# Performance work log

Measured on AMD Instinct MI355X. Metric: run time of the kernel, lower is better.

Reference implementation:

```python
import jax, jax.numpy as jnp
import numpy as np

L, T, F, DIM = 16, 16384, 2, 3
N_MIN, N_MAX = 16.0, 512.0
N_PTS = 262144
# torch code builds np.int32 primes [1, 2654435761, 805459861]; 2654435761 wraps to -1640531535.
# Since T is a power of two, int32 wraparound multiply/xor followed by nonnegative mod T gives
# bit-identical indices to the int64 torch computation.
PIS = jnp.array([1, -1640531535, 805459861], dtype=jnp.int32)
# corner ordering from get_indices: corner k = a*4+b*2+c with a->dim0, b->dim1, c->dim2
OFFS = jnp.array([[(k >> 2) & 1, (k >> 1) & 1, k & 1] for k in range(8)], dtype=jnp.float32)  # (8,3)


def setup_inputs() -> dict:
    key = jax.random.key(0)
    k1, k2 = jax.random.split(key)
    x = jax.random.uniform(k1, (N_PTS, DIM), dtype=jnp.float32)
    # nn.init.uniform_(weight, a=-1e-4, b=1e-4) for each of L tables of shape (T, F)
    embeddings = jax.random.uniform(k2, (L, T, F), minval=-1e-4, maxval=1e-4, dtype=jnp.float32)
    return {"x": x, "embeddings": embeddings}


def reference(x, embeddings):
    # per-level growth factor b = exp((log Nmax - log Nmin)/L); N_l = Nmin * b**l
    b = jnp.exp((jnp.log(N_MAX) - jnp.log(N_MIN)) / L)
    N_l = N_MIN * b ** jnp.arange(L, dtype=jnp.float32)                      # (L,)
    un_x = x[None, :, :] * N_l[:, None, None]                                # (L,N,3)  (mu=0, sigma=1)
    lo = jnp.floor(un_x)
    hi = jnp.ceil(un_x)
    d = hi - lo                                                              # (L,N,3)
    nz = d != 0
    diff = jnp.where(nz, (un_x - lo) / jnp.where(nz, d, 1.0), 0.0)           # (L,N,3)

    mask = OFFS.astype(bool)[None, None]                                     # (1,1,8,3)
    corners = jnp.where(mask, hi[:, :, None, :], lo[:, :, None, :])          # (L,N,8,3)
    ci = corners.astype(jnp.int32)
    prod = ci * PIS                                                          # (L,N,8,3) wrapping int32 mul
    idx = jnp.mod(prod[..., 0] ^ prod[..., 1] ^ prod[..., 2], T)             # (L,N,8)

    # per-level table gather: (L,T,F)[ (L,N,8) ] -> (L,N,8,F)
    feats = jax.vmap(lambda emb, i: emb[i])(embeddings, idx)

    # trilinear weights: prod over dims of (diff if corner bit else 1-diff)
    w = jnp.prod(jnp.where(mask, diff[:, :, None, :], 1.0 - diff[:, :, None, :]), axis=-1)  # (L,N,8)
    c = jnp.einsum('lnc,lncf->lnf', w, feats)                                # (L,N,F)
    return jnp.transpose(c, (1, 0, 2)).reshape(x.shape[0], L * F)            # (N, L*F)
```

## Files before the change

kernel.cpp:

```cpp
#include <hip/hip_runtime.h>
#include <stdint.h>

constexpr int L_LEVELS = 16;
constexpr int T_SIZE   = 16384;
constexpr int N_PTS    = 262144;

typedef _Float16 h2 __attribute__((ext_vector_type(2)));
typedef _Float16 h4 __attribute__((ext_vector_type(4)));
typedef _Float16 h8 __attribute__((ext_vector_type(8)));

constexpr uint32_t P1_4 = 2654435761u * 4u;
constexpr uint32_t P2_4 = 805459861u * 4u;
constexpr uint32_t M4   = (T_SIZE - 1) * 4u;

__device__ __forceinline__ h2 lerp2(h2 a, h2 b, h2 t) {
    return a + t * (b - a);
}

__global__ __launch_bounds__(256) void cvt_emb(
    const float4* __restrict__ src, h4* __restrict__ dst)
{
    const int i = blockIdx.x * 256 + threadIdx.x;
    const float4 v = src[i];
    h4 w = { (_Float16)v.x, (_Float16)v.y, (_Float16)v.z, (_Float16)v.w };
    dst[i] = w;
}

__global__ __launch_bounds__(1024, 4) void hash_encode_pair(
    const float* __restrict__ x,
    const h2* __restrict__ emb16,
    h2* __restrict__ ws)
{
    __shared__ h2 tab[2][T_SIZE];

    const int lp    = blockIdx.x & 7;
    const int chunk = blockIdx.x >> 3;
    const int t     = threadIdx.x;
    const int n0    = chunk * 8192 + t * 8;

    {
        const float4* __restrict__ sA =
            reinterpret_cast<const float4*>(emb16 + (size_t)lp * T_SIZE);
        const float4* __restrict__ sB =
            reinterpret_cast<const float4*>(emb16 + (size_t)(lp + 8) * T_SIZE);
        float4* __restrict__ dA = reinterpret_cast<float4*>(tab[0]);
        float4* __restrict__ dB = reinterpret_cast<float4*>(tab[1]);
#pragma unroll
        for (int it = 0; it < 4; ++it) {
            dA[it * 1024 + t] = sA[it * 1024 + t];
            dB[it * 1024 + t] = sB[it * 1024 + t];
        }
    }

    union { float4 q[6]; float f[24]; } xs;
    {
        const float4* __restrict__ xv =
            reinterpret_cast<const float4*>(x + (size_t)n0 * 3);
#pragma unroll
        for (int i = 0; i < 6; ++i) xs.q[i] = xv[i];
    }

    __syncthreads();

#pragma unroll 1
    for (int s = 0; s < 2; ++s) {
        const int lv = lp + 8 * s;
        const float Nl = 16.0f * exp2f((float)lv * 0.3125f);
        const char* __restrict__ tb = reinterpret_cast<const char*>(tab[s]);

        union { h2 r[8]; float4 q[2]; } res;

#pragma unroll
        for (int p = 0; p < 8; ++p) {
            const float u0 = xs.f[3 * p + 0] * Nl;
            const float u1 = xs.f[3 * p + 1] * Nl;
            const float u2 = xs.f[3 * p + 2] * Nl;

            const float fl0 = floorf(u0), fl1 = floorf(u1), fl2 = floorf(u2);
            const float df0 = u0 - fl0, df1 = u1 - fl1, df2 = u2 - fl2;

            const uint32_t q0 = ((uint32_t)(int32_t)fl0) << 2;
            const uint32_t q1 = ((uint32_t)(int32_t)fl1) * P1_4;
            const uint32_t q2 = ((uint32_t)(int32_t)fl2) * P2_4;
            const uint32_t d0 = (q0 ^ (q0 + 4u))   & M4;
            const uint32_t d1 = (q1 ^ (q1 + P1_4)) & M4;
            const uint32_t d2 = (q2 ^ (q2 + P2_4)) & M4;

            uint32_t off = (q0 ^ q1 ^ q2) & M4;

            constexpr int gray[8] = {0, 1, 3, 2, 6, 7, 5, 4};
            h2 f[8];
#pragma unroll
            for (int j = 0; j < 8; ++j) {
                f[gray[j]] = *reinterpret_cast<const h2*>(tb + off);
                if (j < 7) {
                    const int tog = gray[j] ^ gray[j + 1];
                    off ^= (tog == 4) ? d0 : (tog == 2) ? d1 : d2;
                }
            }

            const _Float16 h0 = (_Float16)df0, h1 = (_Float16)df1,
                           hz = (_Float16)df2;
            const h2 t0 = {h0, h0}, t1 = {h1, h1}, t2 = {hz, hz};
            h2 e0 = lerp2(f[0], f[1], t2);
            h2 e1 = lerp2(f[2], f[3], t2);
            h2 e2 = lerp2(f[4], f[5], t2);
            h2 e3 = lerp2(f[6], f[7], t2);
            h2 g0 = lerp2(e0, e1, t1);
            h2 g1 = lerp2(e2, e3, t1);
            res.r[p] = lerp2(g0, g1, t0);
        }

        float4* ws4 = reinterpret_cast<float4*>(ws + (size_t)lv * N_PTS + n0);
        ws4[0] = res.q[0];
        ws4[1] = res.q[1];
    }
}

__global__ __launch_bounds__(256) void transpose_lnf_nlf(
    const h2* __restrict__ ws,
    float4* __restrict__ out4)
{
    __shared__ h2 tile[L_LEVELS][514];
    const int t    = threadIdx.x;
    const int base = blockIdx.x * 512;

#pragma unroll
    for (int l = 0; l < L_LEVELS; ++l) {
        const float2 v = *reinterpret_cast<const float2*>(
            ws + (size_t)l * N_PTS + base + 2 * t);
        *reinterpret_cast<float2*>(&tile[l][2 * t]) = v;
    }
    __syncthreads();

#pragma unroll
    for (int i = 0; i < L_LEVELS; ++i) {
        const int flat = i * 256 + t;
        const int p  = flat >> 3;
        const int lp = flat & 7;
        h2 a = tile[2 * lp][p];
        h2 b = tile[2 * lp + 1][p];
        float4 o = { (float)a.x, (float)a.y, (float)b.x, (float)b.y };
        out4[(size_t)(base + p) * 8 + lp] = o;
    }
}

__global__ __launch_bounds__(512, 4) void hash_encode_direct(
    const float* __restrict__ x,
    const float* __restrict__ emb,
    float2* __restrict__ out)
{
    __shared__ h2 tab[T_SIZE];

    const int l     = blockIdx.x & (L_LEVELS - 1);
    const int chunk = blockIdx.x >> 4;
    const int t     = threadIdx.x;
    const int n0    = chunk * 4096 + t * 8;

    {
        const float4* __restrict__ src =
            reinterpret_cast<const float4*>(emb + (size_t)l * T_SIZE * 2);
        h8* __restrict__ d8 = reinterpret_cast<h8*>(tab);
#pragma unroll
        for (int it = 0; it < 8; ++it) {
            const int i = it * 512 + t;
            float4 a = src[2 * i];
            float4 b = src[2 * i + 1];
            h8 w = { (_Float16)a.x, (_Float16)a.y, (_Float16)a.z, (_Float16)a.w,
                     (_Float16)b.x, (_Float16)b.y, (_Float16)b.z, (_Float16)b.w };
            d8[i] = w;
        }
    }
    union { float4 q[6]; float f[24]; } xs;
    {
        const float4* __restrict__ xv =
            reinterpret_cast<const float4*>(x + (size_t)n0 * 3);
#pragma unroll
        for (int i = 0; i < 6; ++i) xs.q[i] = xv[i];
    }
    __syncthreads();

    const float Nl = 16.0f * exp2f((float)l * 0.3125f);
    const char* __restrict__ tb = reinterpret_cast<const char*>(tab);

#pragma unroll
    for (int p = 0; p < 8; ++p) {
        const float u0 = xs.f[3 * p + 0] * Nl;
        const float u1 = xs.f[3 * p + 1] * Nl;
        const float u2 = xs.f[3 * p + 2] * Nl;
        const float fl0 = floorf(u0), fl1 = floorf(u1), fl2 = floorf(u2);
        const float df0 = u0 - fl0, df1 = u1 - fl1, df2 = u2 - fl2;
        const uint32_t q0 = ((uint32_t)(int32_t)fl0) << 2;
        const uint32_t q1 = ((uint32_t)(int32_t)fl1) * P1_4;
        const uint32_t q2 = ((uint32_t)(int32_t)fl2) * P2_4;
        const uint32_t d0 = (q0 ^ (q0 + 4u))   & M4;
        const uint32_t d1 = (q1 ^ (q1 + P1_4)) & M4;
        const uint32_t d2 = (q2 ^ (q2 + P2_4)) & M4;
        uint32_t off = (q0 ^ q1 ^ q2) & M4;
        constexpr int gray[8] = {0, 1, 3, 2, 6, 7, 5, 4};
        h2 f[8];
#pragma unroll
        for (int j = 0; j < 8; ++j) {
            f[gray[j]] = *reinterpret_cast<const h2*>(tb + off);
            if (j < 7) {
                const int tog = gray[j] ^ gray[j + 1];
                off ^= (tog == 4) ? d0 : (tog == 2) ? d1 : d2;
            }
        }
        const _Float16 h0 = (_Float16)df0, h1 = (_Float16)df1, hz = (_Float16)df2;
        const h2 t0 = {h0, h0}, t1 = {h1, h1}, t2 = {hz, hz};
        h2 e0 = lerp2(f[0], f[1], t2);
        h2 e1 = lerp2(f[2], f[3], t2);
        h2 e2 = lerp2(f[4], f[5], t2);
        h2 e3 = lerp2(f[6], f[7], t2);
        h2 g0 = lerp2(e0, e1, t1);
        h2 g1 = lerp2(e2, e3, t1);
        h2 r  = lerp2(g0, g1, t0);
        out[(size_t)(n0 + p) * L_LEVELS + l] =
            make_float2((float)r.x, (float)r.y);
    }
}

extern "C" void kernel_launch(void* const* d_in, const int* in_sizes, int n_in,
                              void* d_out, int out_size, void* d_ws, size_t ws_size,
                              hipStream_t stream) {
    const float* x   = (const float*)d_in[0];
    const float* emb = (const float*)d_in[1];

    const size_t ws_arr_bytes = (size_t)N_PTS * L_LEVELS * sizeof(h2);
    const size_t emb16_bytes  = (size_t)L_LEVELS * T_SIZE * sizeof(h2);

    if (ws_size >= ws_arr_bytes + emb16_bytes) {
        h2* ws    = (h2*)d_ws;
        h2* emb16 = (h2*)((char*)d_ws + ws_arr_bytes);

        cvt_emb<<<512, 256, 0, stream>>>(
            (const float4*)emb, (h4*)emb16);
        hash_encode_pair<<<256, 1024, 0, stream>>>(x, emb16, ws);
        transpose_lnf_nlf<<<N_PTS / 512, 256, 0, stream>>>(
            ws, (float4*)d_out);
    } else {
        hash_encode_direct<<<1024, 512, 0, stream>>>(x, emb, (float2*)d_out);
    }
}
```

Before: 88.09 us.

## Use one level per block with smaller LDS table and more blocks

Replaces the paired-level kernel (two 64KB tables, 1024 threads, 256 blocks, 8192 points per block) with one level per block (one 64KB table, 512 threads, 1024 blocks, 4096 points per block). This halves LDS per block, which allows more resident blocks and spreads work over more blocks for better occupancy and load balance. In exchange, each block reads x for only one level, so x traffic and table-staging overhead per point rise.

```diff
diff --git a/kernel.cpp b/kernel.cpp
--- a/kernel.cpp
+++ b/kernel.cpp
@@ -26,30 +26,25 @@
     dst[i] = w;
 }
 
-__global__ __launch_bounds__(1024, 4) void hash_encode_pair(
+__global__ __launch_bounds__(512, 4) void hash_encode_lds(
     const float* __restrict__ x,
     const h2* __restrict__ emb16,
     h2* __restrict__ ws)
 {
-    __shared__ h2 tab[2][T_SIZE];
-
-    const int lp    = blockIdx.x & 7;
-    const int chunk = blockIdx.x >> 3;
+    __shared__ h2 tab[T_SIZE];
+
+    const int l     = blockIdx.x & (L_LEVELS - 1);
+    const int chunk = blockIdx.x >> 4;
     const int t     = threadIdx.x;
-    const int n0    = chunk * 8192 + t * 8;
-
-    {
-        const float4* __restrict__ sA =
-            reinterpret_cast<const float4*>(emb16 + (size_t)lp * T_SIZE);
-        const float4* __restrict__ sB =
-            reinterpret_cast<const float4*>(emb16 + (size_t)(lp + 8) * T_SIZE);
-        float4* __restrict__ dA = reinterpret_cast<float4*>(tab[0]);
-        float4* __restrict__ dB = reinterpret_cast<float4*>(tab[1]);
-#pragma unroll
-        for (int it = 0; it < 4; ++it) {
-            dA[it * 1024 + t] = sA[it * 1024 + t];
-            dB[it * 1024 + t] = sB[it * 1024 + t];
-        }
+    const int n0    = chunk * 4096 + t * 8;
+
+    {
+        const float4* __restrict__ s4 =
+            reinterpret_cast<const float4*>(emb16 + (size_t)l * T_SIZE);
+        float4* __restrict__ d4 = reinterpret_cast<float4*>(tab);
+#pragma unroll
+        for (int it = 0; it < 8; ++it)
+            d4[it * 512 + t] = s4[it * 512 + t];
     }
 
     union { float4 q[6]; float f[24]; } xs;
@@ -62,59 +57,54 @@
 
     __syncthreads();
 
-#pragma unroll 1
-    for (int s = 0; s < 2; ++s) {
-        const int lv = lp + 8 * s;
-        const float Nl = 16.0f * exp2f((float)lv * 0.3125f);
-        const char* __restrict__ tb = reinterpret_cast<const char*>(tab[s]);
-
-        union { h2 r[8]; float4 q[2]; } res;
-
-#pragma unroll
-        for (int p = 0; p < 8; ++p) {
-            const float u0 = xs.f[3 * p + 0] * Nl;
-            const float u1 = xs.f[3 * p + 1] * Nl;
-            const float u2 = xs.f[3 * p + 2] * Nl;
-
-            const float fl0 = floorf(u0), fl1 = floorf(u1), fl2 = floorf(u2);
-            const float df0 = u0 - fl0, df1 = u1 - fl1, df2 = u2 - fl2;
-
-            const uint32_t q0 = ((uint32_t)(int32_t)fl0) << 2;
-            const uint32_t q1 = ((uint32_t)(int32_t)fl1) * P1_4;
-            const uint32_t q2 = ((uint32_t)(int32_t)fl2) * P2_4;
-            const uint32_t d0 = (q0 ^ (q0 + 4u))   & M4;
-            const uint32_t d1 = (q1 ^ (q1 + P1_4)) & M4;
-            const uint32_t d2 = (q2 ^ (q2 + P2_4)) & M4;
-
-            uint32_t off = (q0 ^ q1 ^ q2) & M4;
-
-            constexpr int gray[8] = {0, 1, 3, 2, 6, 7, 5, 4};
-            h2 f[8];
-#pragma unroll
-            for (int j = 0; j < 8; ++j) {
-                f[gray[j]] = *reinterpret_cast<const h2*>(tb + off);
-                if (j < 7) {
-                    const int tog = gray[j] ^ gray[j + 1];
-                    off ^= (tog == 4) ? d0 : (tog == 2) ? d1 : d2;
-                }
+    const float Nl = 16.0f * exp2f((float)l * 0.3125f);
+    const char* __restrict__ tb = reinterpret_cast<const char*>(tab);
+
+    union { h2 r[8]; float4 q[2]; } res;
+
+#pragma unroll
+    for (int p = 0; p < 8; ++p) {
+        const float u0 = xs.f[3 * p + 0] * Nl;
+        const float u1 = xs.f[3 * p + 1] * Nl;
+        const float u2 = xs.f[3 * p + 2] * Nl;
+
+        const float fl0 = floorf(u0), fl1 = floorf(u1), fl2 = floorf(u2);
+        const float df0 = u0 - fl0, df1 = u1 - fl1, df2 = u2 - fl2;
+
+        const uint32_t q0 = ((uint32_t)(int32_t)fl0) << 2;
+        const uint32_t q1 = ((uint32_t)(int32_t)fl1) * P1_4;
+        const uint32_t q2 = ((uint32_t)(int32_t)fl2) * P2_4;
+        const uint32_t d0 = (q0 ^ (q0 + 4u))   & M4;
+        const uint32_t d1 = (q1 ^ (q1 + P1_4)) & M4;
+        const uint32_t d2 = (q2 ^ (q2 + P2_4)) & M4;
+
+        uint32_t off = (q0 ^ q1 ^ q2) & M4;
+
+        constexpr int gray[8] = {0, 1, 3, 2, 6, 7, 5, 4};
+        h2 f[8];
+#pragma unroll
+        for (int j = 0; j < 8; ++j) {
+            f[gray[j]] = *reinterpret_cast<const h2*>(tb + off);
+            if (j < 7) {
+                const int tog = gray[j] ^ gray[j + 1];
+                off ^= (tog == 4) ? d0 : (tog == 2) ? d1 : d2;
             }
-
-            const _Float16 h0 = (_Float16)df0, h1 = (_Float16)df1,
-                           hz = (_Float16)df2;
-            const h2 t0 = {h0, h0}, t1 = {h1, h1}, t2 = {hz, hz};
-            h2 e0 = lerp2(f[0], f[1], t2);
-            h2 e1 = lerp2(f[2], f[3], t2);
-            h2 e2 = lerp2(f[4], f[5], t2);
-            h2 e3 = lerp2(f[6], f[7], t2);
-            h2 g0 = lerp2(e0, e1, t1);
-            h2 g1 = lerp2(e2, e3, t1);
-            res.r[p] = lerp2(g0, g1, t0);
         }
 
-        float4* ws4 = reinterpret_cast<float4*>(ws + (size_t)lv * N_PTS + n0);
-        ws4[0] = res.q[0];
-        ws4[1] = res.q[1];
-    }
+        const _Float16 h0 = (_Float16)df0, h1 = (_Float16)df1, hz = (_Float16)df2;
+        const h2 t0 = {h0, h0}, t1 = {h1, h1}, t2 = {hz, hz};
+        h2 e0 = lerp2(f[0], f[1], t2);
+        h2 e1 = lerp2(f[2], f[3], t2);
+        h2 e2 = lerp2(f[4], f[5], t2);
+        h2 e3 = lerp2(f[6], f[7], t2);
+        h2 g0 = lerp2(e0, e1, t1);
+        h2 g1 = lerp2(e2, e3, t1);
+        res.r[p] = lerp2(g0, g1, t0);
+    }
+
+    float4* ws4 = reinterpret_cast<float4*>(ws + (size_t)l * N_PTS + n0);
+    ws4[0] = res.q[0];
+    ws4[1] = res.q[1];
 }
 
 __global__ __launch_bounds__(256) void transpose_lnf_nlf(
@@ -234,11 +224,9 @@
         h2* ws    = (h2*)d_ws;
         h2* emb16 = (h2*)((char*)d_ws + ws_arr_bytes);
 
-        cvt_emb<<<512, 256, 0, stream>>>(
-            (const float4*)emb, (h4*)emb16);
-        hash_encode_pair<<<256, 1024, 0, stream>>>(x, emb16, ws);
-        transpose_lnf_nlf<<<N_PTS / 512, 256, 0, stream>>>(
-            ws, (float4*)d_out);
+        cvt_emb<<<512, 256, 0, stream>>>((const float4*)emb, (h4*)emb16);
+        hash_encode_lds<<<1024, 512, 0, stream>>>(x, emb16, ws);
+        transpose_lnf_nlf<<<N_PTS / 512, 256, 0, stream>>>(ws, (float4*)d_out);
     } else {
         hash_encode_direct<<<1024, 512, 0, stream>>>(x, emb, (float2*)d_out);
     }
```

Result: no change. 88.32 us (+0.3%).
